# Kernel tuning notes

Measured on AMD Instinct MI355X. Metric: run time of the kernel, lower is better.

Reference implementation:

```python
import jax, jax.numpy as jnp
import numpy as np

NUM_HEADS = 16
HIDDEN = 1024
ATTN_DIM = 64            # per-head q/k dim
HEAD_OUT = 64            # per-head v dim
OUT_DIM = 1024
BATCH, SEQ = 2, 2048


def setup_inputs() -> dict:
    key = jax.random.key(0)
    ks = jax.random.split(key, 9)
    s_in = 1.0 / np.sqrt(HIDDEN)
    s_o = 1.0 / np.sqrt(NUM_HEADS * HEAD_OUT)
    return {
        "x": jax.random.normal(ks[0], (BATCH, SEQ, HIDDEN), dtype=jnp.float32),
        # Linear weights stored [in, out] so y = x @ W + b
        "Wq": jax.random.uniform(ks[1], (HIDDEN, NUM_HEADS * ATTN_DIM), jnp.float32, -s_in, s_in),
        "bq": jax.random.uniform(ks[2], (NUM_HEADS * ATTN_DIM,), jnp.float32, -s_in, s_in),
        "Wk": jax.random.uniform(ks[3], (HIDDEN, NUM_HEADS * ATTN_DIM), jnp.float32, -s_in, s_in),
        "bk": jax.random.uniform(ks[4], (NUM_HEADS * ATTN_DIM,), jnp.float32, -s_in, s_in),
        "Wv": jax.random.uniform(ks[5], (HIDDEN, NUM_HEADS * HEAD_OUT), jnp.float32, -s_in, s_in),
        "bv": jax.random.uniform(ks[6], (HIDDEN, NUM_HEADS * HEAD_OUT)[1:], jnp.float32, -s_in, s_in),
        "Wo": jax.random.uniform(ks[7], (NUM_HEADS * HEAD_OUT, OUT_DIM), jnp.float32, -s_o, s_o),
        "bo": jax.random.uniform(ks[8], (OUT_DIM,), jnp.float32, -s_o, s_o),
    }


def _split_heads(y, h):
    b, s, _ = y.shape
    return y.reshape(b, s, h, -1).transpose(0, 2, 1, 3)  # [b, h, s, d]


def reference(x, Wq, bq, Wk, bk, Wv, bv, Wo, bo):
    h = NUM_HEADS
    q = _split_heads(x @ Wq + bq, h)                    # [b,h,s,dq]
    k = _split_heads(x @ Wk + bk, h)                    # [b,h,s,dq]
    v = _split_heads(x @ Wv + bv, h)                    # [b,h,s,dv]
    scale = 1.0 / jnp.sqrt(jnp.float32(ATTN_DIM))
    # pattern[b,h,i,j] = key_i . query_j  (i=key index, j=query index)
    pattern = jnp.einsum('bhid,bhjd->bhij', k, q) * scale
    # softmax over key axis (dim=-2), matching t.softmax(..., dim=-2)
    prob = jax.nn.softmax(pattern, axis=-2)             # [b,h,key,query]
    # out[b,h,s,d] = sum_i prob[b,h,i,s] * v[b,h,i,d]
    out = jnp.einsum('bhis,bhid->bhsd', prob, v)        # [b,h,s,dv]
    b, _, s, dv = out.shape
    concat = out.transpose(0, 2, 1, 3).reshape(b, s, h * dv)
    return concat @ Wo + bo
```

## Files before the change

### kernel.cpp

```cpp
#include <hip/hip_runtime.h>
#include <cstdint>
#include <cstddef>

using f16   = _Float16;
using f16x4 = __attribute__((ext_vector_type(4))) _Float16;
using f16x8 = __attribute__((ext_vector_type(8))) _Float16;
using f32x4 = __attribute__((ext_vector_type(4))) float;

__device__ __forceinline__ f32x4 mfma16(f16x8 a, f16x8 b, f32x4 c) {
  return __builtin_amdgcn_mfma_f32_16x16x32_f16(a, b, c, 0, 0, 0);
}

__device__ __forceinline__ void gld16(const f16* g, f16* l) {
  __builtin_amdgcn_global_load_lds(
      (__attribute__((address_space(1))) void*)g,
      (__attribute__((address_space(3))) void*)l, 16, 0, 0);
}

constexpr int BATCH = 2, SEQL = 2048, HID = 1024, NH = 16, DH = 64;
constexpr int TOK = BATCH * SEQL;
constexpr int NQKV = 3 * HID;

__global__ __launch_bounds__(256) void k_prep(const float* __restrict__ x,
                                              const float* __restrict__ Wq,
                                              const float* __restrict__ Wk,
                                              const float* __restrict__ Wv,
                                              const float* __restrict__ Wo,
                                              f16* __restrict__ xh,
                                              f16* __restrict__ WT,
                                              f16* __restrict__ WoT) {
  int mat = blockIdx.z;
  if (mat == 4) {
    int blk = blockIdx.y * 32 + blockIdx.x;
    int base = blk * 4096 + threadIdx.x * 4;
#pragma unroll
    for (int j = 0; j < 4; j++) {
      int i = base + j * 1024;
      float4 v = *(const float4*)(x + i);
      f16x4 o = { (f16)v.x, (f16)v.y, (f16)v.z, (f16)v.w };
      *(f16x4*)(xh + i) = o;
    }
    return;
  }
  __shared__ float tile[32][33];
  const float* W = (mat == 0) ? Wq : (mat == 1) ? Wk : (mat == 2) ? Wv : Wo;
  int in0 = blockIdx.x * 32, out0 = blockIdx.y * 32;
  int c = threadIdx.x & 31, r8 = threadIdx.x >> 5;
#pragma unroll
  for (int i = 0; i < 4; i++) {
    int r = r8 + i * 8;
    tile[r][c] = W[(size_t)(in0 + r) * HID + out0 + c];
  }
  __syncthreads();
#pragma unroll
  for (int i = 0; i < 4; i++) {
    int r = r8 + i * 8;
    f16 v = (f16)tile[c][r];
    if (mat == 3) WoT[(size_t)(out0 + r) * HID + in0 + c] = v;
    else          WT[(size_t)(mat * HID + out0 + r) * HID + in0 + c] = v;
  }
}

__global__ __launch_bounds__(256, 2) void k_gemm_qkv(
    const f16* __restrict__ xh, const f16* __restrict__ WT,
    const float* __restrict__ bq, const float* __restrict__ bk,
    const float* __restrict__ bv,
    f16* __restrict__ Qh, f16* __restrict__ Kh, f16* __restrict__ Vp) {
  constexpr int K = HID;
  int m0 = blockIdx.x * 128, n0 = blockIdx.y * 128;
  int tid = threadIdx.x;
  int w = tid >> 6, lane = tid & 63, lr = lane & 15, lq = lane >> 4;
  int wm = w >> 1, wn = w & 1;
  __shared__ f16 Ash[128 * 32];
  __shared__ f16 Bsh[128 * 32];
  f32x4 acc[4][4];
#pragma unroll
  for (int i = 0; i < 4; i++)
#pragma unroll
    for (int j = 0; j < 4; j++) acc[i][j] = (f32x4){0.f, 0.f, 0.f, 0.f};

  int row0 = tid >> 2, seg0 = tid & 3;
  int row1 = (256 + tid) >> 2;
  const f16* Ag0 = xh + (size_t)(m0 + row0) * K + seg0 * 8;
  const f16* Ag1 = xh + (size_t)(m0 + row1) * K + seg0 * 8;
  const f16* Bg0 = WT + (size_t)(n0 + row0) * K + seg0 * 8;
  const f16* Bg1 = WT + (size_t)(n0 + row1) * K + seg0 * 8;

  for (int k0 = 0; k0 < K; k0 += 32) {
    __syncthreads();
    gld16(Ag0 + k0, Ash + tid * 8);
    gld16(Ag1 + k0, Ash + (256 + tid) * 8);
    gld16(Bg0 + k0, Bsh + tid * 8);
    gld16(Bg1 + k0, Bsh + (256 + tid) * 8);
    __syncthreads();
    f16x8 af[4], bfr[4];
#pragma unroll
    for (int mt = 0; mt < 4; mt++)
      af[mt] = *(const f16x8*)(Ash + (wm * 64 + mt * 16 + lr) * 32 + lq * 8);
#pragma unroll
    for (int nt = 0; nt < 4; nt++)
      bfr[nt] = *(const f16x8*)(Bsh + (wn * 64 + nt * 16 + lr) * 32 + lq * 8);
#pragma unroll
    for (int mt = 0; mt < 4; mt++)
#pragma unroll
      for (int nt = 0; nt < 4; nt++)
        acc[mt][nt] = mfma16(af[mt], bfr[nt], acc[mt][nt]);
  }

#pragma unroll
  for (int nt = 0; nt < 4; nt++) {
    int o = n0 + wn * 64 + nt * 16 + lr;
    int sec = o >> 10, o1 = o & 1023, hh = o1 >> 6, dd = o1 & 63;
    float bias = (sec == 0) ? bq[o1] : (sec == 1) ? bk[o1] : bv[o1];
#pragma unroll
    for (int mt = 0; mt < 4; mt++) {
      int t0 = m0 + wm * 64 + mt * 16 + lq * 4;
      int b = t0 >> 11, s0 = t0 & (SEQL - 1);
      size_t bh = (size_t)(b * NH + hh);
      if (sec == 2) {
        f16x4 pv = { (f16)(acc[mt][nt][0] + bias), (f16)(acc[mt][nt][1] + bias),
                     (f16)(acc[mt][nt][2] + bias), (f16)(acc[mt][nt][3] + bias) };
        int pb = (s0 & ~31) | ((s0 & 12) << 1) | ((s0 >> 2) & 4);
        *(f16x4*)(Vp + (bh * DH + dd) * SEQL + pb) = pv;
      } else {
        f16* dst = (sec == 0) ? Qh : Kh;
#pragma unroll
        for (int r = 0; r < 4; r++)
          dst[(bh * SEQL + s0 + r) * DH + dd] = (f16)(acc[mt][nt][r] + bias);
      }
    }
  }
}

__global__ __launch_bounds__(256, 2) void k_attn(const f16* __restrict__ Qh,
                                                 const f16* __restrict__ Kh,
                                                 const f16* __restrict__ Vp,
                                                 f16* __restrict__ Ao) {
  int bh = blockIdx.x;
  int qblk = blockIdx.y;
  int b = bh >> 4, h = bh & 15;
  int tid = threadIdx.x, w = tid >> 6, lane = tid & 63, lr = lane & 15, lq = lane >> 4;

  __shared__ f16 Ksh[2][64 * 72];
  __shared__ f16 Vsh[2][64 * 72];

  f16x8 qf[2][2];
#pragma unroll
  for (int qt = 0; qt < 2; qt++) {
    const f16* Qbase =
        Qh + ((size_t)bh * SEQL + qblk * 128 + w * 32 + qt * 16 + lr) * DH;
#pragma unroll
    for (int ks = 0; ks < 2; ks++) {
      qf[qt][ks] = *(const f16x8*)(Qbase + ks * 32 + lq * 8);
      qf[qt][ks] = qf[qt][ks] * (f16)0.18033688f;
    }
  }

  f32x4 O[2][4];
#pragma unroll
  for (int qt = 0; qt < 2; qt++)
#pragma unroll
    for (int dt = 0; dt < 4; dt++) O[qt][dt] = (f32x4){0.f, 0.f, 0.f, 0.f};
  float lsum[2] = {0.f, 0.f};

  int srow = tid >> 3, sseg = tid & 7, srow1 = srow + 32;
  const f16* Kg0 = Kh + ((size_t)bh * SEQL + srow) * DH + sseg * 8;
  const f16* Kg1 = Kh + ((size_t)bh * SEQL + srow1) * DH + sseg * 8;
  const f16* Vg0 = Vp + ((size_t)bh * DH + srow) * SEQL + sseg * 8;
  const f16* Vg1 = Vp + ((size_t)bh * DH + srow1) * SEQL + sseg * 8;

  uint4 kr0 = *(const uint4*)(Kg0), kr1 = *(const uint4*)(Kg1);
  uint4 vr0 = *(const uint4*)(Vg0), vr1 = *(const uint4*)(Vg1);

  for (int kb = 0; kb < SEQL / 64; kb++) {
    f16* Kp = Ksh[kb & 1];
    f16* Vq = Vsh[kb & 1];
    *(uint4*)(Kp + srow * 72 + sseg * 8) = kr0;
    *(uint4*)(Kp + srow1 * 72 + sseg * 8) = kr1;
    *(uint4*)(Vq + srow * 72 + sseg * 8) = vr0;
    *(uint4*)(Vq + srow1 * 72 + sseg * 8) = vr1;
    if (kb < SEQL / 64 - 1) {
      size_t ko = (size_t)(kb + 1) * 64 * DH;
      int vo = (kb + 1) * 64;
      kr0 = *(const uint4*)(Kg0 + ko);
      kr1 = *(const uint4*)(Kg1 + ko);
      vr0 = *(const uint4*)(Vg0 + vo);
      vr1 = *(const uint4*)(Vg1 + vo);
    }
    __syncthreads();

    f32x4 sacc[2][4];
#pragma unroll
    for (int qt = 0; qt < 2; qt++)
#pragma unroll
      for (int kt = 0; kt < 4; kt++) sacc[qt][kt] = (f32x4){0.f, 0.f, 0.f, 0.f};
#pragma unroll
    for (int ks = 0; ks < 2; ks++) {
#pragma unroll
      for (int kt = 0; kt < 4; kt++) {
        f16x8 kf = *(const f16x8*)(Kp + (kt * 16 + lr) * 72 + ks * 32 + lq * 8);
        sacc[0][kt] = mfma16(kf, qf[0][ks], sacc[0][kt]);
        sacc[1][kt] = mfma16(kf, qf[1][ks], sacc[1][kt]);
      }
    }

    f16x8 pf[2][2];
#pragma unroll
    for (int qt = 0; qt < 2; qt++) {
      float part = 0.f;
#pragma unroll
      for (int kt = 0; kt < 4; kt++) {
        float p0 = __builtin_amdgcn_exp2f(sacc[qt][kt][0]);
        float p1 = __builtin_amdgcn_exp2f(sacc[qt][kt][1]);
        float p2 = __builtin_amdgcn_exp2f(sacc[qt][kt][2]);
        float p3 = __builtin_amdgcn_exp2f(sacc[qt][kt][3]);
        part += (p0 + p1) + (p2 + p3);
        int s = kt >> 1, off = (kt & 1) * 4;
        pf[qt][s][off + 0] = (f16)p0; pf[qt][s][off + 1] = (f16)p1;
        pf[qt][s][off + 2] = (f16)p2; pf[qt][s][off + 3] = (f16)p3;
      }
      lsum[qt] += part;
    }

#pragma unroll
    for (int s = 0; s < 2; s++) {
#pragma unroll
      for (int dt = 0; dt < 4; dt++) {
        f16x8 vf = *(const f16x8*)(Vq + (dt * 16 + lr) * 72 + s * 32 + lq * 8);
        O[0][dt] = mfma16(vf, pf[0][s], O[0][dt]);
        O[1][dt] = mfma16(vf, pf[1][s], O[1][dt]);
      }
    }
  }

#pragma unroll
  for (int qt = 0; qt < 2; qt++) {
    float l1 = lsum[qt] + __shfl_xor(lsum[qt], 16);
    float ltot = l1 + __shfl_xor(l1, 32);
    float inv = 1.0f / ltot;
    int q = qblk * 128 + w * 32 + qt * 16 + lr;
    f16* dst = Ao + ((size_t)b * SEQL + q) * HID + h * DH;
#pragma unroll
    for (int dt = 0; dt < 4; dt++) {
      f16x4 o = { (f16)(O[qt][dt][0] * inv), (f16)(O[qt][dt][1] * inv),
                  (f16)(O[qt][dt][2] * inv), (f16)(O[qt][dt][3] * inv) };
      *(f16x4*)(dst + dt * 16 + lq * 4) = o;
    }
  }
}

__global__ __launch_bounds__(256, 2) void k_gemm_out(const f16* __restrict__ Ah,
                                                     const f16* __restrict__ WoT,
                                                     const float* __restrict__ bo,
                                                     float* __restrict__ out) {
  constexpr int K = HID;
  int m0 = blockIdx.x * 128, n0 = blockIdx.y * 64;
  int tid = threadIdx.x;
  int w = tid >> 6, lane = tid & 63, lr = lane & 15, lq = lane >> 4;
  int wm = w >> 1, wn = w & 1;
  __shared__ f16 Ash[128 * 32];
  __shared__ f16 Bsh[64 * 32];
  f32x4 acc[4][2];
#pragma unroll
  for (int i = 0; i < 4; i++)
#pragma unroll
    for (int j = 0; j < 2; j++) acc[i][j] = (f32x4){0.f, 0.f, 0.f, 0.f};

  int row0 = tid >> 2, seg0 = tid & 3;
  int row1 = (256 + tid) >> 2;
  const f16* Ag0 = Ah + (size_t)(m0 + row0) * K + seg0 * 8;
  const f16* Ag1 = Ah + (size_t)(m0 + row1) * K + seg0 * 8;
  const f16* Bg0 = WoT + (size_t)(n0 + row0) * K + seg0 * 8;

  for (int k0 = 0; k0 < K; k0 += 32) {
    __syncthreads();
    gld16(Ag0 + k0, Ash + tid * 8);
    gld16(Ag1 + k0, Ash + (256 + tid) * 8);
    gld16(Bg0 + k0, Bsh + tid * 8);
    __syncthreads();
    f16x8 af[4], bfr[2];
#pragma unroll
    for (int mt = 0; mt < 4; mt++)
      af[mt] = *(const f16x8*)(Ash + (wm * 64 + mt * 16 + lr) * 32 + lq * 8);
#pragma unroll
    for (int nt = 0; nt < 2; nt++)
      bfr[nt] = *(const f16x8*)(Bsh + (wn * 32 + nt * 16 + lr) * 32 + lq * 8);
#pragma unroll
    for (int mt = 0; mt < 4; mt++)
#pragma unroll
      for (int nt = 0; nt < 2; nt++)
        acc[mt][nt] = mfma16(af[mt], bfr[nt], acc[mt][nt]);
  }

#pragma unroll
  for (int nt = 0; nt < 2; nt++) {
    int o = n0 + wn * 32 + nt * 16 + lr;
    float bias = bo[o];
#pragma unroll
    for (int mt = 0; mt < 4; mt++) {
      int t0 = m0 + wm * 64 + mt * 16 + lq * 4;
#pragma unroll
      for (int r = 0; r < 4; r++)
        out[(size_t)(t0 + r) * HID + o] = acc[mt][nt][r] + bias;
    }
  }
}

extern "C" void kernel_launch(void* const* d_in, const int* in_sizes, int n_in,
                              void* d_out, int out_size, void* d_ws, size_t ws_size,
                              hipStream_t stream) {
  const float* x  = (const float*)d_in[0];
  const float* Wq = (const float*)d_in[1];
  const float* bq = (const float*)d_in[2];
  const float* Wk = (const float*)d_in[3];
  const float* bk = (const float*)d_in[4];
  const float* Wv = (const float*)d_in[5];
  const float* bv = (const float*)d_in[6];
  const float* Wo = (const float*)d_in[7];
  const float* bo = (const float*)d_in[8];

  char* ws = (char*)d_ws;
  f16* xh  = (f16*)(ws + 0);
  f16* WT  = (f16*)(ws + 8388608);
  f16* WoT = (f16*)(ws + 14680064);
  f16* Qh  = (f16*)(ws + 16777216);
  f16* Kh  = (f16*)(ws + 25165824);
  f16* Vp  = (f16*)(ws + 33554432);
  f16* Ao  = (f16*)(ws + 41943040);

  k_prep<<<dim3(32, 32, 5), 256, 0, stream>>>(x, Wq, Wk, Wv, Wo, xh, WT, WoT);
  k_gemm_qkv<<<dim3(TOK / 128, NQKV / 128), 256, 0, stream>>>(xh, WT, bq, bk, bv,
                                                              Qh, Kh, Vp);
  k_attn<<<dim3(BATCH * NH, SEQL / 128), 256, 0, stream>>>(Qh, Kh, Vp, Ao);
  k_gemm_out<<<dim3(TOK / 128, HID / 64), 256, 0, stream>>>(Ao, WoT, bo,
                                                            (float*)d_out);
}
```

Measured before the change: 189.2 us.

## Fuse all stages into one persistent kernel with software grid barriers

```diff
diff --git a/kernel.cpp b/kernel.cpp
--- a/kernel.cpp
+++ b/kernel.cpp
@@ -20,288 +20,299 @@
 constexpr int BATCH = 2, SEQL = 2048, HID = 1024, NH = 16, DH = 64;
 constexpr int TOK = BATCH * SEQL;
 constexpr int NQKV = 3 * HID;
-
-__global__ __launch_bounds__(256) void k_prep(const float* __restrict__ x,
-                                              const float* __restrict__ Wq,
-                                              const float* __restrict__ Wk,
-                                              const float* __restrict__ Wv,
-                                              const float* __restrict__ Wo,
-                                              f16* __restrict__ xh,
-                                              f16* __restrict__ WT,
-                                              f16* __restrict__ WoT) {
-  int mat = blockIdx.z;
-  if (mat == 4) {
-    int blk = blockIdx.y * 32 + blockIdx.x;
-    int base = blk * 4096 + threadIdx.x * 4;
-#pragma unroll
-    for (int j = 0; j < 4; j++) {
+constexpr int NBLK = 512;
+
+__device__ __forceinline__ void grid_barrier(volatile unsigned* cnt,
+                                             volatile unsigned* gen) {
+  __threadfence();
+  __syncthreads();
+  if (threadIdx.x == 0) {
+    unsigned g = *gen;
+    if (atomicAdd((unsigned*)cnt, 1u) == NBLK - 1) {
+      *cnt = 0;
+      __threadfence();
+      *gen = g + 1;
+    } else {
+      while (*gen == g) __builtin_amdgcn_s_sleep(2);
+    }
+  }
+  __syncthreads();
+  __threadfence();
+}
+
+__global__ __launch_bounds__(256, 2) void k_mega(
+    const float* __restrict__ x,
+    const float* __restrict__ Wq, const float* __restrict__ bq,
+    const float* __restrict__ Wk, const float* __restrict__ bk,
+    const float* __restrict__ Wv, const float* __restrict__ bv,
+    const float* __restrict__ Wo, const float* __restrict__ bo,
+    f16* __restrict__ xh, f16* __restrict__ WT, f16* __restrict__ WoT,
+    f16* __restrict__ Qh, f16* __restrict__ Kh, f16* __restrict__ Vp,
+    f16* __restrict__ Ao, float* __restrict__ out, unsigned* bar) {
+  __shared__ union SM {
+    float wt[32][33];
+    struct { f16 A[128 * 32]; f16 B[128 * 32]; } g;
+    struct { f16 K[2][64 * 72]; f16 V[2][64 * 72]; } at;
+    struct { f16 A[128 * 32]; f16 B[64 * 32]; } og;
+  } sm;
+  const int bid = blockIdx.x, tid = threadIdx.x;
+  const int lane = tid & 63, w = tid >> 6, lr = lane & 15, lq = lane >> 4;
+  volatile unsigned* cnt = bar;
+  volatile unsigned* gen = bar + 1;
+
+  {
+    int base = bid * 8192 + tid * 4;
+#pragma unroll
+    for (int j = 0; j < 8; j++) {
       int i = base + j * 1024;
       float4 v = *(const float4*)(x + i);
       f16x4 o = { (f16)v.x, (f16)v.y, (f16)v.z, (f16)v.w };
       *(f16x4*)(xh + i) = o;
     }
-    return;
-  }
-  __shared__ float tile[32][33];
-  const float* W = (mat == 0) ? Wq : (mat == 1) ? Wk : (mat == 2) ? Wv : Wo;
-  int in0 = blockIdx.x * 32, out0 = blockIdx.y * 32;
-  int c = threadIdx.x & 31, r8 = threadIdx.x >> 5;
-#pragma unroll
-  for (int i = 0; i < 4; i++) {
-    int r = r8 + i * 8;
-    tile[r][c] = W[(size_t)(in0 + r) * HID + out0 + c];
-  }
-  __syncthreads();
-#pragma unroll
-  for (int i = 0; i < 4; i++) {
-    int r = r8 + i * 8;
-    f16 v = (f16)tile[c][r];
-    if (mat == 3) WoT[(size_t)(out0 + r) * HID + in0 + c] = v;
-    else          WT[(size_t)(mat * HID + out0 + r) * HID + in0 + c] = v;
-  }
-}
-
-__global__ __launch_bounds__(256, 2) void k_gemm_qkv(
-    const f16* __restrict__ xh, const f16* __restrict__ WT,
-    const float* __restrict__ bq, const float* __restrict__ bk,
-    const float* __restrict__ bv,
-    f16* __restrict__ Qh, f16* __restrict__ Kh, f16* __restrict__ Vp) {
-  constexpr int K = HID;
-  int m0 = blockIdx.x * 128, n0 = blockIdx.y * 128;
-  int tid = threadIdx.x;
-  int w = tid >> 6, lane = tid & 63, lr = lane & 15, lq = lane >> 4;
-  int wm = w >> 1, wn = w & 1;
-  __shared__ f16 Ash[128 * 32];
-  __shared__ f16 Bsh[128 * 32];
-  f32x4 acc[4][4];
-#pragma unroll
-  for (int i = 0; i < 4; i++)
-#pragma unroll
-    for (int j = 0; j < 4; j++) acc[i][j] = (f32x4){0.f, 0.f, 0.f, 0.f};
-
-  int row0 = tid >> 2, seg0 = tid & 3;
-  int row1 = (256 + tid) >> 2;
-  const f16* Ag0 = xh + (size_t)(m0 + row0) * K + seg0 * 8;
-  const f16* Ag1 = xh + (size_t)(m0 + row1) * K + seg0 * 8;
-  const f16* Bg0 = WT + (size_t)(n0 + row0) * K + seg0 * 8;
-  const f16* Bg1 = WT + (size_t)(n0 + row1) * K + seg0 * 8;
-
-  for (int k0 = 0; k0 < K; k0 += 32) {
-    __syncthreads();
-    gld16(Ag0 + k0, Ash + tid * 8);
-    gld16(Ag1 + k0, Ash + (256 + tid) * 8);
-    gld16(Bg0 + k0, Bsh + tid * 8);
-    gld16(Bg1 + k0, Bsh + (256 + tid) * 8);
-    __syncthreads();
-    f16x8 af[4], bfr[4];
-#pragma unroll
-    for (int mt = 0; mt < 4; mt++)
-      af[mt] = *(const f16x8*)(Ash + (wm * 64 + mt * 16 + lr) * 32 + lq * 8);
-#pragma unroll
-    for (int nt = 0; nt < 4; nt++)
-      bfr[nt] = *(const f16x8*)(Bsh + (wn * 64 + nt * 16 + lr) * 32 + lq * 8);
-#pragma unroll
-    for (int mt = 0; mt < 4; mt++)
-#pragma unroll
-      for (int nt = 0; nt < 4; nt++)
-        acc[mt][nt] = mfma16(af[mt], bfr[nt], acc[mt][nt]);
-  }
-
-#pragma unroll
-  for (int nt = 0; nt < 4; nt++) {
-    int o = n0 + wn * 64 + nt * 16 + lr;
-    int sec = o >> 10, o1 = o & 1023, hh = o1 >> 6, dd = o1 & 63;
-    float bias = (sec == 0) ? bq[o1] : (sec == 1) ? bk[o1] : bv[o1];
-#pragma unroll
-    for (int mt = 0; mt < 4; mt++) {
-      int t0 = m0 + wm * 64 + mt * 16 + lq * 4;
-      int b = t0 >> 11, s0 = t0 & (SEQL - 1);
-      size_t bh = (size_t)(b * NH + hh);
-      if (sec == 2) {
-        f16x4 pv = { (f16)(acc[mt][nt][0] + bias), (f16)(acc[mt][nt][1] + bias),
-                     (f16)(acc[mt][nt][2] + bias), (f16)(acc[mt][nt][3] + bias) };
-        int pb = (s0 & ~31) | ((s0 & 12) << 1) | ((s0 >> 2) & 4);
-        *(f16x4*)(Vp + (bh * DH + dd) * SEQL + pb) = pv;
-      } else {
-        f16* dst = (sec == 0) ? Qh : Kh;
+    int c = tid & 31, r8 = tid >> 5;
+    for (int it = 0; it < 8; it++) {
+      int t = bid * 8 + it;
+      int mat = t >> 10, rem = t & 1023;
+      const float* W = (mat == 0) ? Wq : (mat == 1) ? Wk : (mat == 2) ? Wv : Wo;
+      int in0 = (rem & 31) * 32, out0 = (rem >> 5) * 32;
+      __syncthreads();
+#pragma unroll
+      for (int i = 0; i < 4; i++) {
+        int r = r8 + i * 8;
+        sm.wt[r][c] = W[(size_t)(in0 + r) * HID + out0 + c];
+      }
+      __syncthreads();
+#pragma unroll
+      for (int i = 0; i < 4; i++) {
+        int r = r8 + i * 8;
+        f16 v = (f16)sm.wt[c][r];
+        if (mat == 3) WoT[(size_t)(out0 + r) * HID + in0 + c] = v;
+        else          WT[(size_t)(mat * HID + out0 + r) * HID + in0 + c] = v;
+      }
+    }
+  }
+  grid_barrier(cnt, gen);
+
+  {
+    constexpr int K = HID;
+    int wm = w >> 1, wn = w & 1;
+    int row0 = tid >> 2, seg0 = tid & 3, row1 = row0 + 64;
+    for (int t = bid; t < 768; t += NBLK) {
+      int m0 = (t & 31) * 128, n0 = (t >> 5) * 128;
+      const f16* Ag0 = xh + (size_t)(m0 + row0) * K + seg0 * 8;
+      const f16* Ag1 = xh + (size_t)(m0 + row1) * K + seg0 * 8;
+      const f16* Bg0 = WT + (size_t)(n0 + row0) * K + seg0 * 8;
+      const f16* Bg1 = WT + (size_t)(n0 + row1) * K + seg0 * 8;
+      f32x4 acc[4][4];
+#pragma unroll
+      for (int i = 0; i < 4; i++)
+#pragma unroll
+        for (int j = 0; j < 4; j++) acc[i][j] = (f32x4){0.f, 0.f, 0.f, 0.f};
+
+      for (int k0 = 0; k0 < K; k0 += 32) {
+        __syncthreads();
+        gld16(Ag0 + k0, sm.g.A + tid * 8);
+        gld16(Ag1 + k0, sm.g.A + (256 + tid) * 8);
+        gld16(Bg0 + k0, sm.g.B + tid * 8);
+        gld16(Bg1 + k0, sm.g.B + (256 + tid) * 8);
+        __syncthreads();
+        f16x8 af[4], bfr[4];
+#pragma unroll
+        for (int mt = 0; mt < 4; mt++)
+          af[mt] = *(const f16x8*)(sm.g.A + (wm * 64 + mt * 16 + lr) * 32 + lq * 8);
+#pragma unroll
+        for (int nt = 0; nt < 4; nt++)
+          bfr[nt] = *(const f16x8*)(sm.g.B + (wn * 64 + nt * 16 + lr) * 32 + lq * 8);
+#pragma unroll
+        for (int mt = 0; mt < 4; mt++)
+#pragma unroll
+          for (int nt = 0; nt < 4; nt++)
+            acc[mt][nt] = mfma16(af[mt], bfr[nt], acc[mt][nt]);
+      }
+
+#pragma unroll
+      for (int nt = 0; nt < 4; nt++) {
+        int o = n0 + wn * 64 + nt * 16 + lr;
+        int sec = o >> 10, o1 = o & 1023, hh = o1 >> 6, dd = o1 & 63;
+        float bias = (sec == 0) ? bq[o1] : (sec == 1) ? bk[o1] : bv[o1];
+#pragma unroll
+        for (int mt = 0; mt < 4; mt++) {
+          int t0 = m0 + wm * 64 + mt * 16 + lq * 4;
+          int b = t0 >> 11, s0 = t0 & (SEQL - 1);
+          size_t bh = (size_t)(b * NH + hh);
+          if (sec == 2) {
+            f16x4 pv = { (f16)(acc[mt][nt][0] + bias), (f16)(acc[mt][nt][1] + bias),
+                         (f16)(acc[mt][nt][2] + bias), (f16)(acc[mt][nt][3] + bias) };
+            int pb = (s0 & ~31) | ((s0 & 12) << 1) | ((s0 >> 2) & 4);
+            *(f16x4*)(Vp + (bh * DH + dd) * SEQL + pb) = pv;
+          } else {
+            f16* dst = (sec == 0) ? Qh : Kh;
+#pragma unroll
+            for (int r = 0; r < 4; r++)
+              dst[(bh * SEQL + s0 + r) * DH + dd] = (f16)(acc[mt][nt][r] + bias);
+          }
+        }
+      }
+    }
+  }
+  grid_barrier(cnt, gen);
+
+  {
+    int bh = bid & 31;
+    int qblk = bid >> 5;
+    int b = bh >> 4, h = bh & 15;
+
+    f16x8 qf[2][2];
+#pragma unroll
+    for (int qt = 0; qt < 2; qt++) {
+      const f16* Qbase =
+          Qh + ((size_t)bh * SEQL + qblk * 128 + w * 32 + qt * 16 + lr) * DH;
+#pragma unroll
+      for (int ks = 0; ks < 2; ks++) {
+        qf[qt][ks] = *(const f16x8*)(Qbase + ks * 32 + lq * 8);
+        qf[qt][ks] = qf[qt][ks] * (f16)0.18033688f;
+      }
+    }
+
+    f32x4 O[2][4];
+#pragma unroll
+    for (int qt = 0; qt < 2; qt++)
+#pragma unroll
+      for (int dt = 0; dt < 4; dt++) O[qt][dt] = (f32x4){0.f, 0.f, 0.f, 0.f};
+    float lsum[2] = {0.f, 0.f};
+
+    int srow = tid >> 3, sseg = tid & 7, srow1 = srow + 32;
+    const f16* Kg0 = Kh + ((size_t)bh * SEQL + srow) * DH + sseg * 8;
+    const f16* Kg1 = Kh + ((size_t)bh * SEQL + srow1) * DH + sseg * 8;
+    const f16* Vg0 = Vp + ((size_t)bh * DH + srow) * SEQL + sseg * 8;
+    const f16* Vg1 = Vp + ((size_t)bh * DH + srow1) * SEQL + sseg * 8;
+
+    uint4 kr0 = *(const uint4*)(Kg0), kr1 = *(const uint4*)(Kg1);
+    uint4 vr0 = *(const uint4*)(Vg0), vr1 = *(const uint4*)(Vg1);
+
+    for (int kb = 0; kb < SEQL / 64; kb++) {
+      f16* Kp = sm.at.K[kb & 1];
+      f16* Vq = sm.at.V[kb & 1];
+      *(uint4*)(Kp + srow * 72 + sseg * 8) = kr0;
+      *(uint4*)(Kp + srow1 * 72 + sseg * 8) = kr1;
+      *(uint4*)(Vq + srow * 72 + sseg * 8) = vr0;
+      *(uint4*)(Vq + srow1 * 72 + sseg * 8) = vr1;
+      if (kb < SEQL / 64 - 1) {
+        size_t ko = (size_t)(kb + 1) * 64 * DH;
+        int vo = (kb + 1) * 64;
+        kr0 = *(const uint4*)(Kg0 + ko);
+        kr1 = *(const uint4*)(Kg1 + ko);
+        vr0 = *(const uint4*)(Vg0 + vo);
+        vr1 = *(const uint4*)(Vg1 + vo);
+      }
+      __syncthreads();
+
+      f32x4 sacc[2][4];
+#pragma unroll
+      for (int qt = 0; qt < 2; qt++)
+#pragma unroll
+        for (int kt = 0; kt < 4; kt++) sacc[qt][kt] = (f32x4){0.f, 0.f, 0.f, 0.f};
+#pragma unroll
+      for (int ks = 0; ks < 2; ks++) {
+#pragma unroll
+        for (int kt = 0; kt < 4; kt++) {
+          f16x8 kf = *(const f16x8*)(Kp + (kt * 16 + lr) * 72 + ks * 32 + lq * 8);
+          sacc[0][kt] = mfma16(kf, qf[0][ks], sacc[0][kt]);
+          sacc[1][kt] = mfma16(kf, qf[1][ks], sacc[1][kt]);
+        }
+      }
+
+      f16x8 pf[2][2];
+#pragma unroll
+      for (int qt = 0; qt < 2; qt++) {
+        float part = 0.f;
+#pragma unroll
+        for (int kt = 0; kt < 4; kt++) {
+          float p0 = __builtin_amdgcn_exp2f(sacc[qt][kt][0]);
+          float p1 = __builtin_amdgcn_exp2f(sacc[qt][kt][1]);
+          float p2 = __builtin_amdgcn_exp2f(sacc[qt][kt][2]);
+          float p3 = __builtin_amdgcn_exp2f(sacc[qt][kt][3]);
+          part += (p0 + p1) + (p2 + p3);
+          int s = kt >> 1, off = (kt & 1) * 4;
+          pf[qt][s][off + 0] = (f16)p0; pf[qt][s][off + 1] = (f16)p1;
+          pf[qt][s][off + 2] = (f16)p2; pf[qt][s][off + 3] = (f16)p3;
+        }
+        lsum[qt] += part;
+      }
+
+#pragma unroll
+      for (int s = 0; s < 2; s++) {
+#pragma unroll
+        for (int dt = 0; dt < 4; dt++) {
+          f16x8 vf = *(const f16x8*)(Vq + (dt * 16 + lr) * 72 + s * 32 + lq * 8);
+          O[0][dt] = mfma16(vf, pf[0][s], O[0][dt]);
+          O[1][dt] = mfma16(vf, pf[1][s], O[1][dt]);
+        }
+      }
+    }
+
+#pragma unroll
+    for (int qt = 0; qt < 2; qt++) {
+      float l1 = lsum[qt] + __shfl_xor(lsum[qt], 16);
+      float ltot = l1 + __shfl_xor(l1, 32);
+      float inv = 1.0f / ltot;
+      int q = qblk * 128 + w * 32 + qt * 16 + lr;
+      f16* dst = Ao + ((size_t)b * SEQL + q) * HID + h * DH;
+#pragma unroll
+      for (int dt = 0; dt < 4; dt++) {
+        f16x4 o = { (f16)(O[qt][dt][0] * inv), (f16)(O[qt][dt][1] * inv),
+                    (f16)(O[qt][dt][2] * inv), (f16)(O[qt][dt][3] * inv) };
+        *(f16x4*)(dst + dt * 16 + lq * 4) = o;
+      }
+    }
+  }
+  grid_barrier(cnt, gen);
+
+  {
+    constexpr int K = HID;
+    int m0 = (bid & 31) * 128, n0 = (bid >> 5) * 64;
+    int wm = w >> 1, wn = w & 1;
+    int row0 = tid >> 2, seg0 = tid & 3, row1 = row0 + 64;
+    const f16* Ag0 = Ao + (size_t)(m0 + row0) * K + seg0 * 8;
+    const f16* Ag1 = Ao + (size_t)(m0 + row1) * K + seg0 * 8;
+    const f16* Bg0 = WoT + (size_t)(n0 + row0) * K + seg0 * 8;
+    f32x4 acc[4][2];
+#pragma unroll
+    for (int i = 0; i < 4; i++)
+#pragma unroll
+      for (int j = 0; j < 2; j++) acc[i][j] = (f32x4){0.f, 0.f, 0.f, 0.f};
+
+    for (int k0 = 0; k0 < K; k0 += 32) {
+      __syncthreads();
+      gld16(Ag0 + k0, sm.og.A + tid * 8);
+      gld16(Ag1 + k0, sm.og.A + (256 + tid) * 8);
+      gld16(Bg0 + k0, sm.og.B + tid * 8);
+      __syncthreads();
+      f16x8 af[4], bfr[2];
+#pragma unroll
+      for (int mt = 0; mt < 4; mt++)
+        af[mt] = *(const f16x8*)(sm.og.A + (wm * 64 + mt * 16 + lr) * 32 + lq * 8);
+#pragma unroll
+      for (int nt = 0; nt < 2; nt++)
+        bfr[nt] = *(const f16x8*)(sm.og.B + (wn * 32 + nt * 16 + lr) * 32 + lq * 8);
+#pragma unroll
+      for (int mt = 0; mt < 4; mt++)
+#pragma unroll
+        for (int nt = 0; nt < 2; nt++)
+          acc[mt][nt] = mfma16(af[mt], bfr[nt], acc[mt][nt]);
+    }
+
+#pragma unroll
+    for (int nt = 0; nt < 2; nt++) {
+      int o = n0 + wn * 32 + nt * 16 + lr;
+      float bias = bo[o];
+#pragma unroll
+      for (int mt = 0; mt < 4; mt++) {
+        int t0 = m0 + wm * 64 + mt * 16 + lq * 4;
 #pragma unroll
         for (int r = 0; r < 4; r++)
-          dst[(bh * SEQL + s0 + r) * DH + dd] = (f16)(acc[mt][nt][r] + bias);
-      }
-    }
-  }
-}
-
-__global__ __launch_bounds__(256, 2) void k_attn(const f16* __restrict__ Qh,
-                                                 const f16* __restrict__ Kh,
-                                                 const f16* __restrict__ Vp,
-                                                 f16* __restrict__ Ao) {
-  int bh = blockIdx.x;
-  int qblk = blockIdx.y;
-  int b = bh >> 4, h = bh & 15;
-  int tid = threadIdx.x, w = tid >> 6, lane = tid & 63, lr = lane & 15, lq = lane >> 4;
-
-  __shared__ f16 Ksh[2][64 * 72];
-  __shared__ f16 Vsh[2][64 * 72];
-
-  f16x8 qf[2][2];
-#pragma unroll
-  for (int qt = 0; qt < 2; qt++) {
-    const f16* Qbase =
-        Qh + ((size_t)bh * SEQL + qblk * 128 + w * 32 + qt * 16 + lr) * DH;
-#pragma unroll
-    for (int ks = 0; ks < 2; ks++) {
-      qf[qt][ks] = *(const f16x8*)(Qbase + ks * 32 + lq * 8);
-      qf[qt][ks] = qf[qt][ks] * (f16)0.18033688f;
-    }
-  }
-
-  f32x4 O[2][4];
-#pragma unroll
-  for (int qt = 0; qt < 2; qt++)
-#pragma unroll
-    for (int dt = 0; dt < 4; dt++) O[qt][dt] = (f32x4){0.f, 0.f, 0.f, 0.f};
-  float lsum[2] = {0.f, 0.f};
-
-  int srow = tid >> 3, sseg = tid & 7, srow1 = srow + 32;
-  const f16* Kg0 = Kh + ((size_t)bh * SEQL + srow) * DH + sseg * 8;
-  const f16* Kg1 = Kh + ((size_t)bh * SEQL + srow1) * DH + sseg * 8;
-  const f16* Vg0 = Vp + ((size_t)bh * DH + srow) * SEQL + sseg * 8;
-  const f16* Vg1 = Vp + ((size_t)bh * DH + srow1) * SEQL + sseg * 8;
-
-  uint4 kr0 = *(const uint4*)(Kg0), kr1 = *(const uint4*)(Kg1);
-  uint4 vr0 = *(const uint4*)(Vg0), vr1 = *(const uint4*)(Vg1);
-
-  for (int kb = 0; kb < SEQL / 64; kb++) {
-    f16* Kp = Ksh[kb & 1];
-    f16* Vq = Vsh[kb & 1];
-    *(uint4*)(Kp + srow * 72 + sseg * 8) = kr0;
-    *(uint4*)(Kp + srow1 * 72 + sseg * 8) = kr1;
-    *(uint4*)(Vq + srow * 72 + sseg * 8) = vr0;
-    *(uint4*)(Vq + srow1 * 72 + sseg * 8) = vr1;
-    if (kb < SEQL / 64 - 1) {
-      size_t ko = (size_t)(kb + 1) * 64 * DH;
-      int vo = (kb + 1) * 64;
-      kr0 = *(const uint4*)(Kg0 + ko);
-      kr1 = *(const uint4*)(Kg1 + ko);
-      vr0 = *(const uint4*)(Vg0 + vo);
-      vr1 = *(const uint4*)(Vg1 + vo);
-    }
-    __syncthreads();
-
-    f32x4 sacc[2][4];
-#pragma unroll
-    for (int qt = 0; qt < 2; qt++)
-#pragma unroll
-      for (int kt = 0; kt < 4; kt++) sacc[qt][kt] = (f32x4){0.f, 0.f, 0.f, 0.f};
-#pragma unroll
-    for (int ks = 0; ks < 2; ks++) {
-#pragma unroll
-      for (int kt = 0; kt < 4; kt++) {
-        f16x8 kf = *(const f16x8*)(Kp + (kt * 16 + lr) * 72 + ks * 32 + lq * 8);
-        sacc[0][kt] = mfma16(kf, qf[0][ks], sacc[0][kt]);
-        sacc[1][kt] = mfma16(kf, qf[1][ks], sacc[1][kt]);
-      }
-    }
-
-    f16x8 pf[2][2];
-#pragma unroll
-    for (int qt = 0; qt < 2; qt++) {
-      float part = 0.f;
-#pragma unroll
-      for (int kt = 0; kt < 4; kt++) {
-        float p0 = __builtin_amdgcn_exp2f(sacc[qt][kt][0]);
-        float p1 = __builtin_amdgcn_exp2f(sacc[qt][kt][1]);
-        float p2 = __builtin_amdgcn_exp2f(sacc[qt][kt][2]);
-        float p3 = __builtin_amdgcn_exp2f(sacc[qt][kt][3]);
-        part += (p0 + p1) + (p2 + p3);
-        int s = kt >> 1, off = (kt & 1) * 4;
-        pf[qt][s][off + 0] = (f16)p0; pf[qt][s][off + 1] = (f16)p1;
-        pf[qt][s][off + 2] = (f16)p2; pf[qt][s][off + 3] = (f16)p3;
-      }
-      lsum[qt] += part;
-    }
-
-#pragma unroll
-    for (int s = 0; s < 2; s++) {
-#pragma unroll
-      for (int dt = 0; dt < 4; dt++) {
-        f16x8 vf = *(const f16x8*)(Vq + (dt * 16 + lr) * 72 + s * 32 + lq * 8);
-        O[0][dt] = mfma16(vf, pf[0][s], O[0][dt]);
-        O[1][dt] = mfma16(vf, pf[1][s], O[1][dt]);
-      }
-    }
-  }
-
-#pragma unroll
-  for (int qt = 0; qt < 2; qt++) {
-    float l1 = lsum[qt] + __shfl_xor(lsum[qt], 16);
-    float ltot = l1 + __shfl_xor(l1, 32);
-    float inv = 1.0f / ltot;
-    int q = qblk * 128 + w * 32 + qt * 16 + lr;
-    f16* dst = Ao + ((size_t)b * SEQL + q) * HID + h * DH;
-#pragma unroll
-    for (int dt = 0; dt < 4; dt++) {
-      f16x4 o = { (f16)(O[qt][dt][0] * inv), (f16)(O[qt][dt][1] * inv),
-                  (f16)(O[qt][dt][2] * inv), (f16)(O[qt][dt][3] * inv) };
-      *(f16x4*)(dst + dt * 16 + lq * 4) = o;
-    }
-  }
-}
-
-__global__ __launch_bounds__(256, 2) void k_gemm_out(const f16* __restrict__ Ah,
-                                                     const f16* __restrict__ WoT,
-                                                     const float* __restrict__ bo,
-                                                     float* __restrict__ out) {
-  constexpr int K = HID;
-  int m0 = blockIdx.x * 128, n0 = blockIdx.y * 64;
-  int tid = threadIdx.x;
-  int w = tid >> 6, lane = tid & 63, lr = lane & 15, lq = lane >> 4;
-  int wm = w >> 1, wn = w & 1;
-  __shared__ f16 Ash[128 * 32];
-  __shared__ f16 Bsh[64 * 32];
-  f32x4 acc[4][2];
-#pragma unroll
-  for (int i = 0; i < 4; i++)
-#pragma unroll
-    for (int j = 0; j < 2; j++) acc[i][j] = (f32x4){0.f, 0.f, 0.f, 0.f};
-
-  int row0 = tid >> 2, seg0 = tid & 3;
-  int row1 = (256 + tid) >> 2;
-  const f16* Ag0 = Ah + (size_t)(m0 + row0) * K + seg0 * 8;
-  const f16* Ag1 = Ah + (size_t)(m0 + row1) * K + seg0 * 8;
-  const f16* Bg0 = WoT + (size_t)(n0 + row0) * K + seg0 * 8;
-
-  for (int k0 = 0; k0 < K; k0 += 32) {
-    __syncthreads();
-    gld16(Ag0 + k0, Ash + tid * 8);
-    gld16(Ag1 + k0, Ash + (256 + tid) * 8);
-    gld16(Bg0 + k0, Bsh + tid * 8);
-    __syncthreads();
-    f16x8 af[4], bfr[2];
-#pragma unroll
-    for (int mt = 0; mt < 4; mt++)
-      af[mt] = *(const f16x8*)(Ash + (wm * 64 + mt * 16 + lr) * 32 + lq * 8);
-#pragma unroll
-    for (int nt = 0; nt < 2; nt++)
-      bfr[nt] = *(const f16x8*)(Bsh + (wn * 32 + nt * 16 + lr) * 32 + lq * 8);
-#pragma unroll
-    for (int mt = 0; mt < 4; mt++)
-#pragma unroll
-      for (int nt = 0; nt < 2; nt++)
-        acc[mt][nt] = mfma16(af[mt], bfr[nt], acc[mt][nt]);
-  }
-
-#pragma unroll
-  for (int nt = 0; nt < 2; nt++) {
-    int o = n0 + wn * 32 + nt * 16 + lr;
-    float bias = bo[o];
-#pragma unroll
-    for (int mt = 0; mt < 4; mt++) {
-      int t0 = m0 + wm * 64 + mt * 16 + lq * 4;
-#pragma unroll
-      for (int r = 0; r < 4; r++)
-        out[(size_t)(t0 + r) * HID + o] = acc[mt][nt][r] + bias;
+          out[(size_t)(t0 + r) * HID + o] = acc[mt][nt][r] + bias;
+      }
     }
   }
 }
@@ -327,11 +338,10 @@
   f16* Kh  = (f16*)(ws + 25165824);
   f16* Vp  = (f16*)(ws + 33554432);
   f16* Ao  = (f16*)(ws + 41943040);
-
-  k_prep<<<dim3(32, 32, 5), 256, 0, stream>>>(x, Wq, Wk, Wv, Wo, xh, WT, WoT);
-  k_gemm_qkv<<<dim3(TOK / 128, NQKV / 128), 256, 0, stream>>>(xh, WT, bq, bk, bv,
-                                                              Qh, Kh, Vp);
-  k_attn<<<dim3(BATCH * NH, SEQL / 128), 256, 0, stream>>>(Qh, Kh, Vp, Ao);
-  k_gemm_out<<<dim3(TOK / 128, HID / 64), 256, 0, stream>>>(Ao, WoT, bo,
-                                                            (float*)d_out);
-}
+  float*    out = (float*)d_out;
+  unsigned* bar = (unsigned*)d_out;
+
+  hipMemsetAsync(d_out, 0, 16, stream);
+  k_mega<<<NBLK, 256, 0, stream>>>(x, Wq, bq, Wk, bk, Wv, bv, Wo, bo,
+                                   xh, WT, WoT, Qh, Kh, Vp, Ao, out, bar);
+}
```

After: 628.2 us. 232% more time.
